# Kernel tuning notes

Measured on AMD Instinct MI355X. Metric: run time of the kernel, lower is better.

## Reference

```python
import jax, jax.numpy as jnp
import numpy as np

N = 50000      # nodes
E = 400000     # edges (avg degree 8)
N_IN = 256     # n_in_chan
N_HID = 256    # n_hid_chan


def gcn_conv(x, src, dst, W, b, n):
    """PyG GCNConv: D^{-1/2}(A+I)D^{-1/2} X W^T + b (add_self_loops=True, unit weights)."""
    h = x @ W.T                                           # [n, out]
    # degree over A + I: each node has a self loop (the initial ones) plus in-edges
    deg = jnp.ones((n,), h.dtype).at[dst].add(1.0)        # [n]
    dinv = jax.lax.rsqrt(deg)                             # deg >= 1 always
    norm = dinv[src] * dinv[dst]                          # [E]
    agg = jnp.zeros_like(h).at[dst].add(h[src] * norm[:, None])
    agg = agg + h * (dinv * dinv)[:, None]                # self-loop term, norm = dinv_i^2
    return agg + b


def setup_inputs() -> dict:
    key = jax.random.key(0)
    k1, k2, k3, k4 = jax.random.split(key, 4)
    x = jax.random.normal(k1, (N, N_IN + N_HID), dtype=jnp.float32)
    edge_index = jax.random.randint(k2, (2, E), 0, N, dtype=jnp.int64)
    s1 = 1.0 / np.sqrt(N_IN + N_HID)
    s2 = 1.0 / np.sqrt(N_HID)
    W1 = jax.random.normal(k3, (N_HID, N_IN + N_HID), dtype=jnp.float32) * s1
    W2 = jax.random.normal(k4, (N_HID, N_HID), dtype=jnp.float32) * s2
    b1 = jnp.zeros((N_HID,), jnp.float32)
    b2 = jnp.zeros((N_HID,), jnp.float32)
    return {"x": x, "edge_index": edge_index, "W1": W1, "b1": b1, "W2": W2, "b2": b2}


def reference(x, edge_index, W1, b1, W2, b2):
    src, dst = edge_index[0], edge_index[1]
    h = jax.nn.relu(gcn_conv(x, src, dst, W1, b1, N))
    return gcn_conv(h, src, dst, W2, b2, N)
```

## Files before the change

### kernel.cpp

```cpp
#include <hip/hip_runtime.h>
#include <hip/hip_bf16.h>

#define NN 50000
#define CH 256
#define SLOTS 96
#define G1K 512
#define G2K 256

typedef unsigned short u16;
typedef unsigned int   u32;

using short8 = __attribute__((ext_vector_type(8))) short;
using u16x8  = __attribute__((ext_vector_type(8))) unsigned short;
using f32x4  = __attribute__((ext_vector_type(4))) float;

static __device__ __forceinline__ float4 ld4(const float* p){ return *(const float4*)p; }

static __device__ __forceinline__ u16 f2b(float f){
  u32 u = __float_as_uint(f);
  u = (u + 0x7fffu + ((u >> 16) & 1u)) >> 16;
  return (u16)u;
}
static __device__ __forceinline__ float b2f(u16 b){
  return __uint_as_float(((u32)b) << 16);
}
static __device__ __forceinline__ int pkbf(float lo, float hi){
  __hip_bfloat162 h = __float22bfloat162_rn(make_float2(lo, hi));
  int r; __builtin_memcpy(&r, &h, 4); return r;
}

static __device__ __forceinline__ void gload_lds16(const u16* g, u16* l){
  __builtin_amdgcn_global_load_lds((const __attribute__((address_space(1))) void*)g,
                                   (__attribute__((address_space(3))) void*)l, 16, 0, 0);
}

#define WBAR(vm) do{ \
    asm volatile("s_waitcnt vmcnt(" #vm ") lgkmcnt(0)" ::: "memory"); \
    __builtin_amdgcn_s_barrier(); \
  }while(0)


__global__ void ell_build_kernel(const int* __restrict__ src, const int* __restrict__ dst,
                                 int* __restrict__ deg, int* __restrict__ ell, int E,
                                 const float* __restrict__ W1, u16* __restrict__ W1bf, int w1n4,
                                 const float* __restrict__ W2, u16* __restrict__ W2bf, int w2n4){
  int T = gridDim.x * 256;
  int g = blockIdx.x*256 + threadIdx.x;
  if (g < E){
    int d = dst[g];
    int pos = atomicAdd(&deg[d], 1);
    if (pos < SLOTS) ell[(size_t)d*SLOTS + pos] = src[g];
  }
  for (int i = g; i < w1n4; i += T){
    float4 v = ld4(W1 + (size_t)i*4);
    ushort4 o; o.x=f2b(v.x); o.y=f2b(v.y); o.z=f2b(v.z); o.w=f2b(v.w);
    *(ushort4*)(W1bf + (size_t)i*4) = o;
  }
  for (int i = g; i < w2n4; i += T){
    float4 v = ld4(W2 + (size_t)i*4);
    ushort4 o; o.x=f2b(v.x); o.y=f2b(v.y); o.z=f2b(v.z); o.w=f2b(v.w);
    *(ushort4*)(W2bf + (size_t)i*4) = o;
  }
}


#define G1_GLB(kt, bb) gload_lds16(gb + (kt)*32, &Bs[bb][wave*512])

#define G1_LA(S, k0) do{ \
    A##S##a = ld4(ga + (k0)); A##S##b = ld4(ga + (k0) + 4); \
  }while(0)

#define G1_SA(S) do{ \
    int4 _w = { pkbf(A##S##a.x,A##S##a.y), pkbf(A##S##a.z,A##S##a.w), \
                pkbf(A##S##b.x,A##S##b.y), pkbf(A##S##b.z,A##S##b.w) }; \
    *(int4*)&As[S][aoff] = _w; \
  }while(0)

#define G1_COMP(ra, rb) do{ \
    short8 af[4], bq[2]; \
    _Pragma("unroll") \
    for (int i=0;i<4;i++) af[i] = *(const short8*)&As[ra][(wm*64 + i*16 + lm)*32 + lk]; \
    _Pragma("unroll") \
    for (int j=0;j<2;j++) bq[j] = *(const short8*)&Bs[rb][(wn*32 + j*16 + lm)*32 + lk]; \
    _Pragma("unroll") \
    for (int i=0;i<4;i++) \
      _Pragma("unroll") \
      for (int j=0;j<2;j++) \
        acc[i][j] = __builtin_amdgcn_mfma_f32_16x16x32_bf16(af[i], bq[j], acc[i][j], 0, 0, 0); \
  }while(0)

__global__ __launch_bounds__(512, 4) void gemm1_kernel(const float* __restrict__ A,
                                                       const u16* __restrict__ Bbf,
                                                       u16* __restrict__ C, int M){
  __shared__ u16 As[2][128*32];
  __shared__ u16 Bs[4][128*32];
  int tid = threadIdx.x;
  int wave = tid >> 6, lane = tid & 63;
  int bm = blockIdx.x, bn = blockIdx.y;

  int sr = tid >> 2;
  int sc = (tid & 3) * 8;
  int ar = bm*128 + sr; if (ar > M-1) ar = M-1;
  const float* ga = A + (size_t)ar*G1K + sc;
  const u16*   gb = Bbf + (size_t)(bn*128 + sr)*G1K + sc;
  int aoff = sr*32 + sc;

  int wm = wave & 1, wn = wave >> 1;
  int lm = lane & 15;
  int lk = (lane >> 4) * 8;

  f32x4 acc[4][2] = {};

  float4 A0a,A0b;
  float4 A1a,A1b;

  G1_LA(0, 0);
  G1_GLB(0, 0);
  G1_LA(1, 32);
  G1_GLB(1, 1);
  G1_SA(0);
  G1_LA(0, 64);
  asm volatile("s_waitcnt vmcnt(0) lgkmcnt(0)" ::: "memory");
  __builtin_amdgcn_s_barrier();

  G1_GLB( 2,2); G1_COMP(0,0); G1_SA(1); G1_LA(1, 96); WBAR(3);
  G1_GLB( 3,3); G1_COMP(1,1); G1_SA(0); G1_LA(0,128); WBAR(3);
  G1_GLB( 4,0); G1_COMP(0,2); G1_SA(1); G1_LA(1,160); WBAR(3);
  G1_GLB( 5,1); G1_COMP(1,3); G1_SA(0); G1_LA(0,192); WBAR(3);
  G1_GLB( 6,2); G1_COMP(0,0); G1_SA(1); G1_LA(1,224); WBAR(3);
  G1_GLB( 7,3); G1_COMP(1,1); G1_SA(0); G1_LA(0,256); WBAR(3);
  G1_GLB( 8,0); G1_COMP(0,2); G1_SA(1); G1_LA(1,288); WBAR(3);
  G1_GLB( 9,1); G1_COMP(1,3); G1_SA(0); G1_LA(0,320); WBAR(3);
  G1_GLB(10,2); G1_COMP(0,0); G1_SA(1); G1_LA(1,352); WBAR(3);
  G1_GLB(11,3); G1_COMP(1,1); G1_SA(0); G1_LA(0,384); WBAR(3);
  G1_GLB(12,0); G1_COMP(0,2); G1_SA(1); G1_LA(1,416); WBAR(3);
  G1_GLB(13,1); G1_COMP(1,3); G1_SA(0); G1_LA(0,448); WBAR(3);
  G1_GLB(14,2); G1_COMP(0,0); G1_SA(1); G1_LA(1,480); WBAR(3);
  G1_GLB(15,3); G1_COMP(1,1); G1_SA(0);               WBAR(1);
                G1_COMP(0,2); G1_SA(1);               WBAR(0);
                G1_COMP(1,3);

  int rb = (lane >> 4) * 4;
  #pragma unroll
  for (int i=0;i<4;i++){
    #pragma unroll
    for (int r=0;r<4;r++){
      int row = bm*128 + wm*64 + i*16 + rb + r;
      if (row < M){
        #pragma unroll
        for (int j=0;j<2;j++){
          int col = bn*128 + wn*32 + j*16 + lm;
          C[(size_t)row*CH + col] = f2b(acc[i][j][r]);
        }
      }
    }
  }
}


#define G2_GLB(kt, bb) do{ \
    gload_lds16(ga + (kt)*32, &As2[bb][wave*512]); \
    gload_lds16(gb + (kt)*32, &Bs2[bb][wave*512]); \
  }while(0)

#define G2_COMP(rb) do{ \
    short8 af[4], bq[2]; \
    _Pragma("unroll") \
    for (int i=0;i<4;i++) af[i] = *(const short8*)&As2[rb][(wm*64 + i*16 + lm)*32 + lk]; \
    _Pragma("unroll") \
    for (int j=0;j<2;j++) bq[j] = *(const short8*)&Bs2[rb][(wn*32 + j*16 + lm)*32 + lk]; \
    _Pragma("unroll") \
    for (int i=0;i<4;i++) \
      _Pragma("unroll") \
      for (int j=0;j<2;j++) \
        acc[i][j] = __builtin_amdgcn_mfma_f32_16x16x32_bf16(af[i], bq[j], acc[i][j], 0, 0, 0); \
  }while(0)

__global__ __launch_bounds__(512, 4) void gemm2_kernel(const u16* __restrict__ A,
                                                       const u16* __restrict__ B,
                                                       u16* __restrict__ C, int M){
  __shared__ u16 As2[4][128*32];
  __shared__ u16 Bs2[4][128*32];
  int tid = threadIdx.x;
  int wave = tid >> 6, lane = tid & 63;
  int bm = blockIdx.x, bn = blockIdx.y;

  int sr = tid >> 2;
  int sc = (tid & 3) * 8;
  int ar = bm*128 + sr; if (ar > M-1) ar = M-1;
  const u16* ga = A + (size_t)ar*G2K + sc;
  const u16* gb = B + (size_t)(bn*128 + sr)*G2K + sc;

  int wm = wave & 1, wn = wave >> 1;
  int lm = lane & 15;
  int lk = (lane >> 4) * 8;

  f32x4 acc[4][2] = {};

  G2_GLB(0, 0);
  G2_GLB(1, 1);
  asm volatile("s_waitcnt vmcnt(0)" ::: "memory");
  __builtin_amdgcn_s_barrier();

  G2_GLB(2, 2); G2_COMP(0); WBAR(2);
  G2_GLB(3, 3); G2_COMP(1); WBAR(2);
  G2_GLB(4, 0); G2_COMP(2); WBAR(2);
  G2_GLB(5, 1); G2_COMP(3); WBAR(2);
  G2_GLB(6, 2); G2_COMP(0); WBAR(2);
  G2_GLB(7, 3); G2_COMP(1); WBAR(2);
                G2_COMP(2); WBAR(0);
                G2_COMP(3);

  int rb = (lane >> 4) * 4;
  #pragma unroll
  for (int i=0;i<4;i++){
    #pragma unroll
    for (int r=0;r<4;r++){
      int row = bm*128 + wm*64 + i*16 + rb + r;
      if (row < M){
        #pragma unroll
        for (int j=0;j<2;j++){
          int col = bn*128 + wn*32 + j*16 + lm;
          C[(size_t)row*CH + col] = f2b(acc[i][j][r]);
        }
      }
    }
  }
}


template<bool RELU, bool OUTBF>
__global__ __launch_bounds__(256) void aggregate_kernel(const u16* __restrict__ h,
                                                        const float* __restrict__ bias,
                                                        const int* __restrict__ deg,
                                                        const int* __restrict__ ell,
                                                        void* __restrict__ outv, int n){
  int wave = threadIdx.x >> 6;
  int lane = threadIdx.x & 63;
  int i = blockIdx.x*4 + wave;
  if (i >= n) return;
  int half = lane >> 5;
  int c = (lane & 31) * 8;

  int degi = deg[i];
  float di = rsqrtf(1.0f + (float)degi);
  int m = degi < SLOTS ? degi : SLOTS;
  const int* row = ell + (size_t)i*SLOTS;

  float acc[8];
  #pragma unroll
  for (int k=0;k<8;k++) acc[k] = 0.f;

  int e = half;
  for (; e + 6 < m; e += 8){
    int s0 = row[e],   s1 = row[e+2], s2 = row[e+4], s3 = row[e+6];
    float n0 = rsqrtf(1.0f + (float)deg[s0]) * di;
    float n1 = rsqrtf(1.0f + (float)deg[s1]) * di;
    float n2 = rsqrtf(1.0f + (float)deg[s2]) * di;
    float n3 = rsqrtf(1.0f + (float)deg[s3]) * di;
    u16x8 h0 = *(const u16x8*)(h + (size_t)s0*CH + c);
    u16x8 h1 = *(const u16x8*)(h + (size_t)s1*CH + c);
    u16x8 h2 = *(const u16x8*)(h + (size_t)s2*CH + c);
    u16x8 h3 = *(const u16x8*)(h + (size_t)s3*CH + c);
    #pragma unroll
    for (int k=0;k<8;k++) acc[k] += b2f(h0[k])*n0;
    #pragma unroll
    for (int k=0;k<8;k++) acc[k] += b2f(h1[k])*n1;
    #pragma unroll
    for (int k=0;k<8;k++) acc[k] += b2f(h2[k])*n2;
    #pragma unroll
    for (int k=0;k<8;k++) acc[k] += b2f(h3[k])*n3;
  }
  for (; e < m; e += 2){
    int s0 = row[e];
    float n0 = rsqrtf(1.0f + (float)deg[s0]) * di;
    u16x8 h0 = *(const u16x8*)(h + (size_t)s0*CH + c);
    #pragma unroll
    for (int k=0;k<8;k++) acc[k] += b2f(h0[k])*n0;
  }

  if (half == 0){
    float w = di*di;
    float4 b0 = ld4(bias + c), b1 = ld4(bias + c + 4);
    u16x8 hv = *(const u16x8*)(h + (size_t)i*CH + c);
    acc[0] += b2f(hv[0])*w + b0.x; acc[1] += b2f(hv[1])*w + b0.y;
    acc[2] += b2f(hv[2])*w + b0.z; acc[3] += b2f(hv[3])*w + b0.w;
    acc[4] += b2f(hv[4])*w + b1.x; acc[5] += b2f(hv[5])*w + b1.y;
    acc[6] += b2f(hv[6])*w + b1.z; acc[7] += b2f(hv[7])*w + b1.w;
  }

  #pragma unroll
  for (int k=0;k<8;k++) acc[k] += __shfl_xor(acc[k], 32, 64);

  if (half == 0){
    if (RELU){
      #pragma unroll
      for (int k=0;k<8;k++) acc[k] = fmaxf(acc[k], 0.f);
    }
    if (OUTBF){
      u16x8 o;
      #pragma unroll
      for (int k=0;k<8;k++) o[k] = f2b(acc[k]);
      *(u16x8*)((u16*)outv + (size_t)i*CH + c) = o;
    } else {
      float* op = (float*)outv + (size_t)i*CH + c;
      *(float4*)op       = make_float4(acc[0],acc[1],acc[2],acc[3]);
      *(float4*)(op + 4) = make_float4(acc[4],acc[5],acc[6],acc[7]);
    }
  }
}


extern "C" void kernel_launch(void* const* d_in, const int* in_sizes, int n_in,
                              void* d_out, int out_size, void* d_ws, size_t ws_size,
                              hipStream_t stream){
  const float* x  = (const float*)d_in[0];
  const int*   ei = (const int*)d_in[1];
  const float* W1 = (const float*)d_in[2];
  const float* b1 = (const float*)d_in[3];
  const float* W2 = (const float*)d_in[4];
  const float* b2 = (const float*)d_in[5];
  float* out = (float*)d_out;

  const int n = NN;
  const int E = in_sizes[1] / 2;
  const int* src = ei;
  const int* dst = ei + E;

  char* ws = (char*)d_ws;
  size_t off = 0;
  auto alloc = [&](size_t bytes)->char* {
    char* p = ws + off;
    off += (bytes + 255) & ~(size_t)255;
    return p;
  };
  u16*   h1bf   = (u16*)  alloc((size_t)n*CH*sizeof(u16));
  u16*   g2out  = (u16*)  alloc((size_t)n*CH*sizeof(u16));
  u16*   W1bf   = (u16*)  alloc((size_t)CH*G1K*sizeof(u16));
  u16*   W2bf   = (u16*)  alloc((size_t)CH*CH*sizeof(u16));
  int*   deg    = (int*)  alloc((size_t)n*sizeof(int));
  int*   ell    = (int*)  alloc((size_t)n*SLOTS*sizeof(int));
  (void)ws_size;

  u16* g1out = (u16*)d_out;

  hipMemsetAsync(deg, 0, (size_t)n*sizeof(int), stream);
  ell_build_kernel<<<(E+255)/256, 256, 0, stream>>>(src, dst, deg, ell, E,
                                                    W1, W1bf, CH*G1K/4,
                                                    W2, W2bf, CH*CH/4);

  dim3 gg((n+127)/128, CH/128);
  gemm1_kernel<<<gg, 512, 0, stream>>>(x, W1bf, g1out, n);
  aggregate_kernel<true, true><<<(n+3)/4, 256, 0, stream>>>(g1out, b1, deg, ell, h1bf, n);

  gemm2_kernel<<<gg, 512, 0, stream>>>(h1bf, W2bf, g2out, n);
  aggregate_kernel<false, false><<<(n+3)/4, 256, 0, stream>>>(g2out, b2, deg, ell, out, n);
}
```

Measured before the change: 313.4 us.

## Retile GEMMs to 64x256 blocks with full-width N per block

```diff
diff --git a/kernel.cpp b/kernel.cpp
--- a/kernel.cpp
+++ b/kernel.cpp
@@ -64,7 +64,12 @@
 }
 
 
-#define G1_GLB(kt, bb) gload_lds16(gb + (kt)*32, &Bs[bb][wave*512])
+#define G1_GLB(kt, bb) do{ \
+    gload_lds16(gB + (size_t)(kt)*32,               &Bs[bb][wave*2048]); \
+    gload_lds16(gB + (size_t)(kt)*32 + 16*G1K,      &Bs[bb][wave*2048 + 512]); \
+    gload_lds16(gB + (size_t)(kt)*32 + 32*G1K,      &Bs[bb][wave*2048 + 1024]); \
+    gload_lds16(gB + (size_t)(kt)*32 + 48*G1K,      &Bs[bb][wave*2048 + 1536]); \
+  }while(0)
 
 #define G1_LA(S, k0) do{ \
     A##S##a = ld4(ga + (k0)); A##S##b = ld4(ga + (k0) + 4); \
@@ -77,79 +82,77 @@
   }while(0)
 
 #define G1_COMP(ra, rb) do{ \
-    short8 af[4], bq[2]; \
-    _Pragma("unroll") \
-    for (int i=0;i<4;i++) af[i] = *(const short8*)&As[ra][(wm*64 + i*16 + lm)*32 + lk]; \
-    _Pragma("unroll") \
-    for (int j=0;j<2;j++) bq[j] = *(const short8*)&Bs[rb][(wn*32 + j*16 + lm)*32 + lk]; \
+    short8 af[4], bq[4]; \
+    _Pragma("unroll") \
+    for (int i=0;i<4;i++) af[i] = *(const short8*)&As[ra][(i*16 + lm)*32 + lk]; \
+    _Pragma("unroll") \
+    for (int j=0;j<4;j++) bq[j] = *(const short8*)&Bs[rb][(wave*64 + j*16 + lm)*32 + lk]; \
     _Pragma("unroll") \
     for (int i=0;i<4;i++) \
       _Pragma("unroll") \
-      for (int j=0;j<2;j++) \
+      for (int j=0;j<4;j++) \
         acc[i][j] = __builtin_amdgcn_mfma_f32_16x16x32_bf16(af[i], bq[j], acc[i][j], 0, 0, 0); \
   }while(0)
 
-__global__ __launch_bounds__(512, 4) void gemm1_kernel(const float* __restrict__ A,
+__global__ __launch_bounds__(256, 4) void gemm1_kernel(const float* __restrict__ A,
                                                        const u16* __restrict__ Bbf,
                                                        u16* __restrict__ C, int M){
-  __shared__ u16 As[2][128*32];
-  __shared__ u16 Bs[4][128*32];
+  __shared__ u16 As[2][64*32];
+  __shared__ u16 Bs[2][256*32];
   int tid = threadIdx.x;
   int wave = tid >> 6, lane = tid & 63;
-  int bm = blockIdx.x, bn = blockIdx.y;
-
-  int sr = tid >> 2;
-  int sc = (tid & 3) * 8;
-  int ar = bm*128 + sr; if (ar > M-1) ar = M-1;
-  const float* ga = A + (size_t)ar*G1K + sc;
-  const u16*   gb = Bbf + (size_t)(bn*128 + sr)*G1K + sc;
-  int aoff = sr*32 + sc;
-
-  int wm = wave & 1, wn = wave >> 1;
+  int bm = blockIdx.x;
+
+  int sra = tid >> 2;
+  int sca = (tid & 3) * 8;
+  int ar = bm*64 + sra; if (ar > M-1) ar = M-1;
+  const float* ga = A + (size_t)ar*G1K + sca;
+  int aoff = sra*32 + sca;
+  const u16* gB = Bbf + (size_t)(wave*64 + (lane>>2))*G1K + (lane&3)*8;
+
   int lm = lane & 15;
   int lk = (lane >> 4) * 8;
 
-  f32x4 acc[4][2] = {};
+  f32x4 acc[4][4] = {};
 
   float4 A0a,A0b;
   float4 A1a,A1b;
 
+  G1_GLB(0, 0);
   G1_LA(0, 0);
-  G1_GLB(0, 0);
   G1_LA(1, 32);
-  G1_GLB(1, 1);
   G1_SA(0);
   G1_LA(0, 64);
   asm volatile("s_waitcnt vmcnt(0) lgkmcnt(0)" ::: "memory");
   __builtin_amdgcn_s_barrier();
 
-  G1_GLB( 2,2); G1_COMP(0,0); G1_SA(1); G1_LA(1, 96); WBAR(3);
-  G1_GLB( 3,3); G1_COMP(1,1); G1_SA(0); G1_LA(0,128); WBAR(3);
-  G1_GLB( 4,0); G1_COMP(0,2); G1_SA(1); G1_LA(1,160); WBAR(3);
-  G1_GLB( 5,1); G1_COMP(1,3); G1_SA(0); G1_LA(0,192); WBAR(3);
-  G1_GLB( 6,2); G1_COMP(0,0); G1_SA(1); G1_LA(1,224); WBAR(3);
-  G1_GLB( 7,3); G1_COMP(1,1); G1_SA(0); G1_LA(0,256); WBAR(3);
-  G1_GLB( 8,0); G1_COMP(0,2); G1_SA(1); G1_LA(1,288); WBAR(3);
-  G1_GLB( 9,1); G1_COMP(1,3); G1_SA(0); G1_LA(0,320); WBAR(3);
-  G1_GLB(10,2); G1_COMP(0,0); G1_SA(1); G1_LA(1,352); WBAR(3);
-  G1_GLB(11,3); G1_COMP(1,1); G1_SA(0); G1_LA(0,384); WBAR(3);
-  G1_GLB(12,0); G1_COMP(0,2); G1_SA(1); G1_LA(1,416); WBAR(3);
-  G1_GLB(13,1); G1_COMP(1,3); G1_SA(0); G1_LA(0,448); WBAR(3);
-  G1_GLB(14,2); G1_COMP(0,0); G1_SA(1); G1_LA(1,480); WBAR(3);
-  G1_GLB(15,3); G1_COMP(1,1); G1_SA(0);               WBAR(1);
-                G1_COMP(0,2); G1_SA(1);               WBAR(0);
-                G1_COMP(1,3);
+  G1_GLB( 1,1); G1_COMP(0,0); G1_SA(1); G1_LA(1, 96); WBAR(2);
+  G1_GLB( 2,0); G1_COMP(1,1); G1_SA(0); G1_LA(0,128); WBAR(2);
+  G1_GLB( 3,1); G1_COMP(0,0); G1_SA(1); G1_LA(1,160); WBAR(2);
+  G1_GLB( 4,0); G1_COMP(1,1); G1_SA(0); G1_LA(0,192); WBAR(2);
+  G1_GLB( 5,1); G1_COMP(0,0); G1_SA(1); G1_LA(1,224); WBAR(2);
+  G1_GLB( 6,0); G1_COMP(1,1); G1_SA(0); G1_LA(0,256); WBAR(2);
+  G1_GLB( 7,1); G1_COMP(0,0); G1_SA(1); G1_LA(1,288); WBAR(2);
+  G1_GLB( 8,0); G1_COMP(1,1); G1_SA(0); G1_LA(0,320); WBAR(2);
+  G1_GLB( 9,1); G1_COMP(0,0); G1_SA(1); G1_LA(1,352); WBAR(2);
+  G1_GLB(10,0); G1_COMP(1,1); G1_SA(0); G1_LA(0,384); WBAR(2);
+  G1_GLB(11,1); G1_COMP(0,0); G1_SA(1); G1_LA(1,416); WBAR(2);
+  G1_GLB(12,0); G1_COMP(1,1); G1_SA(0); G1_LA(0,448); WBAR(2);
+  G1_GLB(13,1); G1_COMP(0,0); G1_SA(1); G1_LA(1,480); WBAR(2);
+  G1_GLB(14,0); G1_COMP(1,1); G1_SA(0);               WBAR(0);
+  G1_GLB(15,1); G1_COMP(0,0); G1_SA(1);               WBAR(0);
+                G1_COMP(1,1);
 
   int rb = (lane >> 4) * 4;
   #pragma unroll
   for (int i=0;i<4;i++){
     #pragma unroll
     for (int r=0;r<4;r++){
-      int row = bm*128 + wm*64 + i*16 + rb + r;
+      int row = bm*64 + i*16 + rb + r;
       if (row < M){
         #pragma unroll
-        for (int j=0;j<2;j++){
-          int col = bn*128 + wn*32 + j*16 + lm;
+        for (int j=0;j<4;j++){
+          int col = wave*64 + j*16 + lm;
           C[(size_t)row*CH + col] = f2b(acc[i][j][r]);
         }
       }
@@ -159,68 +162,67 @@
 
 
 #define G2_GLB(kt, bb) do{ \
-    gload_lds16(ga + (kt)*32, &As2[bb][wave*512]); \
-    gload_lds16(gb + (kt)*32, &Bs2[bb][wave*512]); \
+    gload_lds16(gA + (size_t)(kt)*32,          &As2[bb][wave*512]); \
+    gload_lds16(gB + (size_t)(kt)*32,          &Bs2[bb][wave*2048]); \
+    gload_lds16(gB + (size_t)(kt)*32 + 16*G2K, &Bs2[bb][wave*2048 + 512]); \
+    gload_lds16(gB + (size_t)(kt)*32 + 32*G2K, &Bs2[bb][wave*2048 + 1024]); \
+    gload_lds16(gB + (size_t)(kt)*32 + 48*G2K, &Bs2[bb][wave*2048 + 1536]); \
   }while(0)
 
 #define G2_COMP(rb) do{ \
-    short8 af[4], bq[2]; \
-    _Pragma("unroll") \
-    for (int i=0;i<4;i++) af[i] = *(const short8*)&As2[rb][(wm*64 + i*16 + lm)*32 + lk]; \
-    _Pragma("unroll") \
-    for (int j=0;j<2;j++) bq[j] = *(const short8*)&Bs2[rb][(wn*32 + j*16 + lm)*32 + lk]; \
+    short8 af[4], bq[4]; \
+    _Pragma("unroll") \
+    for (int i=0;i<4;i++) af[i] = *(const short8*)&As2[rb][(i*16 + lm)*32 + lk]; \
+    _Pragma("unroll") \
+    for (int j=0;j<4;j++) bq[j] = *(const short8*)&Bs2[rb][(wave*64 + j*16 + lm)*32 + lk]; \
     _Pragma("unroll") \
     for (int i=0;i<4;i++) \
       _Pragma("unroll") \
-      for (int j=0;j<2;j++) \
+      for (int j=0;j<4;j++) \
         acc[i][j] = __builtin_amdgcn_mfma_f32_16x16x32_bf16(af[i], bq[j], acc[i][j], 0, 0, 0); \
   }while(0)
 
-__global__ __launch_bounds__(512, 4) void gemm2_kernel(const u16* __restrict__ A,
+__global__ __launch_bounds__(256, 4) void gemm2_kernel(const u16* __restrict__ A,
                                                        const u16* __restrict__ B,
                                                        u16* __restrict__ C, int M){
-  __shared__ u16 As2[4][128*32];
-  __shared__ u16 Bs2[4][128*32];
+  __shared__ u16 As2[2][64*32];
+  __shared__ u16 Bs2[2][256*32];
   int tid = threadIdx.x;
   int wave = tid >> 6, lane = tid & 63;
-  int bm = blockIdx.x, bn = blockIdx.y;
-
-  int sr = tid >> 2;
-  int sc = (tid & 3) * 8;
-  int ar = bm*128 + sr; if (ar > M-1) ar = M-1;
-  const u16* ga = A + (size_t)ar*G2K + sc;
-  const u16* gb = B + (size_t)(bn*128 + sr)*G2K + sc;
-
-  int wm = wave & 1, wn = wave >> 1;
+  int bm = blockIdx.x;
+
+  int ar = bm*64 + wave*16 + (lane>>2); if (ar > M-1) ar = M-1;
+  const u16* gA = A + (size_t)ar*G2K + (lane&3)*8;
+  const u16* gB = B + (size_t)(wave*64 + (lane>>2))*G2K + (lane&3)*8;
+
   int lm = lane & 15;
   int lk = (lane >> 4) * 8;
 
-  f32x4 acc[4][2] = {};
+  f32x4 acc[4][4] = {};
 
   G2_GLB(0, 0);
-  G2_GLB(1, 1);
   asm volatile("s_waitcnt vmcnt(0)" ::: "memory");
   __builtin_amdgcn_s_barrier();
 
-  G2_GLB(2, 2); G2_COMP(0); WBAR(2);
-  G2_GLB(3, 3); G2_COMP(1); WBAR(2);
-  G2_GLB(4, 0); G2_COMP(2); WBAR(2);
-  G2_GLB(5, 1); G2_COMP(3); WBAR(2);
-  G2_GLB(6, 2); G2_COMP(0); WBAR(2);
-  G2_GLB(7, 3); G2_COMP(1); WBAR(2);
-                G2_COMP(2); WBAR(0);
-                G2_COMP(3);
+  G2_GLB(1, 1); G2_COMP(0); WBAR(0);
+  G2_GLB(2, 0); G2_COMP(1); WBAR(0);
+  G2_GLB(3, 1); G2_COMP(0); WBAR(0);
+  G2_GLB(4, 0); G2_COMP(1); WBAR(0);
+  G2_GLB(5, 1); G2_COMP(0); WBAR(0);
+  G2_GLB(6, 0); G2_COMP(1); WBAR(0);
+  G2_GLB(7, 1); G2_COMP(0); WBAR(0);
+                G2_COMP(1);
 
   int rb = (lane >> 4) * 4;
   #pragma unroll
   for (int i=0;i<4;i++){
     #pragma unroll
     for (int r=0;r<4;r++){
-      int row = bm*128 + wm*64 + i*16 + rb + r;
+      int row = bm*64 + i*16 + rb + r;
       if (row < M){
         #pragma unroll
-        for (int j=0;j<2;j++){
-          int col = bn*128 + wn*32 + j*16 + lm;
+        for (int j=0;j<4;j++){
+          int col = wave*64 + j*16 + lm;
           C[(size_t)row*CH + col] = f2b(acc[i][j][r]);
         }
       }
@@ -349,10 +351,10 @@
                                                     W1, W1bf, CH*G1K/4,
                                                     W2, W2bf, CH*CH/4);
 
-  dim3 gg((n+127)/128, CH/128);
-  gemm1_kernel<<<gg, 512, 0, stream>>>(x, W1bf, g1out, n);
+  dim3 gg((n+63)/64);
+  gemm1_kernel<<<gg, 256, 0, stream>>>(x, W1bf, g1out, n);
   aggregate_kernel<true, true><<<(n+3)/4, 256, 0, stream>>>(g1out, b1, deg, ell, h1bf, n);
 
-  gemm2_kernel<<<gg, 512, 0, stream>>>(h1bf, W2bf, g2out, n);
+  gemm2_kernel<<<gg, 256, 0, stream>>>(h1bf, W2bf, g2out, n);
   aggregate_kernel<false, false><<<(n+3)/4, 256, 0, stream>>>(g2out, b2, deg, ell, out, n);
 }
```

After: 316.9 us. No clear change (+1.1%).

## Fold degree normalization into GEMM epilogues and aggregate before second GEMM

Applied to the files above, without the earlier changes.

```diff
diff --git a/kernel.cpp b/kernel.cpp
--- a/kernel.cpp
+++ b/kernel.cpp
@@ -29,7 +29,7 @@
   int r; __builtin_memcpy(&r, &h, 4); return r;
 }
 
-static __device__ __forceinline__ void gload_lds16(const u16* g, u16* l){
+static __device__ __forceinline__ void gload_lds16(const void* g, void* l){
   __builtin_amdgcn_global_load_lds((const __attribute__((address_space(1))) void*)g,
                                    (__attribute__((address_space(3))) void*)l, 16, 0, 0);
 }
@@ -53,18 +53,18 @@
   }
   for (int i = g; i < w1n4; i += T){
     float4 v = ld4(W1 + (size_t)i*4);
-    ushort4 o; o.x=f2b(v.x); o.y=f2b(v.y); o.z=f2b(v.z); o.w=f2b(v.w);
-    *(ushort4*)(W1bf + (size_t)i*4) = o;
+    int2 o = { pkbf(v.x,v.y), pkbf(v.z,v.w) };
+    *(int2*)(W1bf + (size_t)i*4) = o;
   }
   for (int i = g; i < w2n4; i += T){
     float4 v = ld4(W2 + (size_t)i*4);
-    ushort4 o; o.x=f2b(v.x); o.y=f2b(v.y); o.z=f2b(v.z); o.w=f2b(v.w);
-    *(ushort4*)(W2bf + (size_t)i*4) = o;
-  }
-}
-
-
-#define G1_GLB(kt, bb) gload_lds16(gb + (kt)*32, &Bs[bb][wave*512])
+    int2 o = { pkbf(v.x,v.y), pkbf(v.z,v.w) };
+    *(int2*)(W2bf + (size_t)i*4) = o;
+  }
+}
+
+
+#define G1_GLB(kt, bb) gload_lds16(gb + (size_t)(kt)*32, &Bs[bb][wave*512])
 
 #define G1_LA(S, k0) do{ \
     A##S##a = ld4(ga + (k0)); A##S##b = ld4(ga + (k0) + 4); \
@@ -91,6 +91,7 @@
 
 __global__ __launch_bounds__(512, 4) void gemm1_kernel(const float* __restrict__ A,
                                                        const u16* __restrict__ Bbf,
+                                                       const int* __restrict__ deg,
                                                        u16* __restrict__ C, int M){
   __shared__ u16 As[2][128*32];
   __shared__ u16 Bs[4][128*32];
@@ -147,10 +148,11 @@
     for (int r=0;r<4;r++){
       int row = bm*128 + wm*64 + i*16 + rb + r;
       if (row < M){
+        float dr = rsqrtf(1.0f + (float)deg[row]);
         #pragma unroll
         for (int j=0;j<2;j++){
           int col = bn*128 + wn*32 + j*16 + lm;
-          C[(size_t)row*CH + col] = f2b(acc[i][j][r]);
+          C[(size_t)row*CH + col] = f2b(acc[i][j][r] * dr);
         }
       }
     }
@@ -159,8 +161,8 @@
 
 
 #define G2_GLB(kt, bb) do{ \
-    gload_lds16(ga + (kt)*32, &As2[bb][wave*512]); \
-    gload_lds16(gb + (kt)*32, &Bs2[bb][wave*512]); \
+    gload_lds16(ga + (size_t)(kt)*32, &As2[bb][wave*512]); \
+    gload_lds16(gb + (size_t)(kt)*32, &Bs2[bb][wave*512]); \
   }while(0)
 
 #define G2_COMP(rb) do{ \
@@ -178,7 +180,8 @@
 
 __global__ __launch_bounds__(512, 4) void gemm2_kernel(const u16* __restrict__ A,
                                                        const u16* __restrict__ B,
-                                                       u16* __restrict__ C, int M){
+                                                       float* __restrict__ Cout,
+                                                       const float* __restrict__ bias, int M){
   __shared__ u16 As2[4][128*32];
   __shared__ u16 Bs2[4][128*32];
   int tid = threadIdx.x;
@@ -210,6 +213,10 @@
   G2_GLB(7, 3); G2_COMP(1); WBAR(2);
                 G2_COMP(2); WBAR(0);
                 G2_COMP(3);
+
+  float bv[2];
+  #pragma unroll
+  for (int j=0;j<2;j++) bv[j] = bias[bn*128 + wn*32 + j*16 + lm];
 
   int rb = (lane >> 4) * 4;
   #pragma unroll
@@ -221,7 +228,7 @@
         #pragma unroll
         for (int j=0;j<2;j++){
           int col = bn*128 + wn*32 + j*16 + lm;
-          C[(size_t)row*CH + col] = f2b(acc[i][j][r]);
+          Cout[(size_t)row*CH + col] = acc[i][j][r] + bv[j];
         }
       }
     }
@@ -229,85 +236,85 @@
 }
 
 
-template<bool RELU, bool OUTBF>
+#define AGG_G(u, s) ushort4 hg##u = *(const ushort4*)(h + (size_t)(s)*CH + c)
+#define AGG_ACC(u) do{ a0 += b2f(hg##u.x); a1 += b2f(hg##u.y); \
+                       a2 += b2f(hg##u.z); a3 += b2f(hg##u.w); }while(0)
+
+template<bool RELU, bool BIAS, bool SCALEOUT>
 __global__ __launch_bounds__(256) void aggregate_kernel(const u16* __restrict__ h,
                                                         const float* __restrict__ bias,
                                                         const int* __restrict__ deg,
                                                         const int* __restrict__ ell,
-                                                        void* __restrict__ outv, int n){
+                                                        u16* __restrict__ outv, int n){
   int wave = threadIdx.x >> 6;
   int lane = threadIdx.x & 63;
   int i = blockIdx.x*4 + wave;
   if (i >= n) return;
-  int half = lane >> 5;
-  int c = (lane & 31) * 8;
+  i = __builtin_amdgcn_readfirstlane(i);
 
   int degi = deg[i];
   float di = rsqrtf(1.0f + (float)degi);
   int m = degi < SLOTS ? degi : SLOTS;
-  const int* row = ell + (size_t)i*SLOTS;
-
-  float acc[8];
-  #pragma unroll
-  for (int k=0;k<8;k++) acc[k] = 0.f;
-
-  int e = half;
-  for (; e + 6 < m; e += 8){
-    int s0 = row[e],   s1 = row[e+2], s2 = row[e+4], s3 = row[e+6];
-    float n0 = rsqrtf(1.0f + (float)deg[s0]) * di;
-    float n1 = rsqrtf(1.0f + (float)deg[s1]) * di;
-    float n2 = rsqrtf(1.0f + (float)deg[s2]) * di;
-    float n3 = rsqrtf(1.0f + (float)deg[s3]) * di;
-    u16x8 h0 = *(const u16x8*)(h + (size_t)s0*CH + c);
-    u16x8 h1 = *(const u16x8*)(h + (size_t)s1*CH + c);
-    u16x8 h2 = *(const u16x8*)(h + (size_t)s2*CH + c);
-    u16x8 h3 = *(const u16x8*)(h + (size_t)s3*CH + c);
-    #pragma unroll
-    for (int k=0;k<8;k++) acc[k] += b2f(h0[k])*n0;
-    #pragma unroll
-    for (int k=0;k<8;k++) acc[k] += b2f(h1[k])*n1;
-    #pragma unroll
-    for (int k=0;k<8;k++) acc[k] += b2f(h2[k])*n2;
-    #pragma unroll
-    for (int k=0;k<8;k++) acc[k] += b2f(h3[k])*n3;
-  }
-  for (; e < m; e += 2){
-    int s0 = row[e];
-    float n0 = rsqrtf(1.0f + (float)deg[s0]) * di;
-    u16x8 h0 = *(const u16x8*)(h + (size_t)s0*CH + c);
-    #pragma unroll
-    for (int k=0;k<8;k++) acc[k] += b2f(h0[k])*n0;
-  }
-
-  if (half == 0){
-    float w = di*di;
-    float4 b0 = ld4(bias + c), b1 = ld4(bias + c + 4);
-    u16x8 hv = *(const u16x8*)(h + (size_t)i*CH + c);
-    acc[0] += b2f(hv[0])*w + b0.x; acc[1] += b2f(hv[1])*w + b0.y;
-    acc[2] += b2f(hv[2])*w + b0.z; acc[3] += b2f(hv[3])*w + b0.w;
-    acc[4] += b2f(hv[4])*w + b1.x; acc[5] += b2f(hv[5])*w + b1.y;
-    acc[6] += b2f(hv[6])*w + b1.z; acc[7] += b2f(hv[7])*w + b1.w;
-  }
-
-  #pragma unroll
-  for (int k=0;k<8;k++) acc[k] += __shfl_xor(acc[k], 32, 64);
-
-  if (half == 0){
-    if (RELU){
-      #pragma unroll
-      for (int k=0;k<8;k++) acc[k] = fmaxf(acc[k], 0.f);
-    }
-    if (OUTBF){
-      u16x8 o;
-      #pragma unroll
-      for (int k=0;k<8;k++) o[k] = f2b(acc[k]);
-      *(u16x8*)((u16*)outv + (size_t)i*CH + c) = o;
-    } else {
-      float* op = (float*)outv + (size_t)i*CH + c;
-      *(float4*)op       = make_float4(acc[0],acc[1],acc[2],acc[3]);
-      *(float4*)(op + 4) = make_float4(acc[4],acc[5],acc[6],acc[7]);
-    }
-  }
+  const int* __restrict__ row = ell + (size_t)i*SLOTS;
+  int vidx = row[lane];
+  int c = lane * 4;
+
+  float a0=0.f, a1=0.f, a2=0.f, a3=0.f;
+
+  int m64 = m < 64 ? m : 64;
+  int nb = m64 >> 3;
+  for (int b = 0; b < nb; ++b){
+    int base = b*8;
+    int s0=__shfl(vidx,base  ), s1=__shfl(vidx,base+1), s2=__shfl(vidx,base+2), s3=__shfl(vidx,base+3);
+    int s4=__shfl(vidx,base+4), s5=__shfl(vidx,base+5), s6=__shfl(vidx,base+6), s7=__shfl(vidx,base+7);
+    AGG_G(0,s0); AGG_G(1,s1); AGG_G(2,s2); AGG_G(3,s3);
+    AGG_G(4,s4); AGG_G(5,s5); AGG_G(6,s6); AGG_G(7,s7);
+    AGG_ACC(0); AGG_ACC(1); AGG_ACC(2); AGG_ACC(3);
+    AGG_ACC(4); AGG_ACC(5); AGG_ACC(6); AGG_ACC(7);
+  }
+  int base = nb*8;
+  if (base < m64){
+    int t0 = base   < m64 ? __shfl(vidx,base  ) : i;  float w0 = base   < m64 ? 1.f : 0.f;
+    int t1 = base+1 < m64 ? __shfl(vidx,base+1) : i;  float w1 = base+1 < m64 ? 1.f : 0.f;
+    int t2 = base+2 < m64 ? __shfl(vidx,base+2) : i;  float w2 = base+2 < m64 ? 1.f : 0.f;
+    int t3 = base+3 < m64 ? __shfl(vidx,base+3) : i;  float w3 = base+3 < m64 ? 1.f : 0.f;
+    int t4 = base+4 < m64 ? __shfl(vidx,base+4) : i;  float w4 = base+4 < m64 ? 1.f : 0.f;
+    int t5 = base+5 < m64 ? __shfl(vidx,base+5) : i;  float w5 = base+5 < m64 ? 1.f : 0.f;
+    int t6 = base+6 < m64 ? __shfl(vidx,base+6) : i;  float w6 = base+6 < m64 ? 1.f : 0.f;
+    int t7 = base+7 < m64 ? __shfl(vidx,base+7) : i;  float w7 = base+7 < m64 ? 1.f : 0.f;
+    AGG_G(0,t0); AGG_G(1,t1); AGG_G(2,t2); AGG_G(3,t3);
+    AGG_G(4,t4); AGG_G(5,t5); AGG_G(6,t6); AGG_G(7,t7);
+    a0 += b2f(hg0.x)*w0 + b2f(hg1.x)*w1 + b2f(hg2.x)*w2 + b2f(hg3.x)*w3
+        + b2f(hg4.x)*w4 + b2f(hg5.x)*w5 + b2f(hg6.x)*w6 + b2f(hg7.x)*w7;
+    a1 += b2f(hg0.y)*w0 + b2f(hg1.y)*w1 + b2f(hg2.y)*w2 + b2f(hg3.y)*w3
+        + b2f(hg4.y)*w4 + b2f(hg5.y)*w5 + b2f(hg6.y)*w6 + b2f(hg7.y)*w7;
+    a2 += b2f(hg0.z)*w0 + b2f(hg1.z)*w1 + b2f(hg2.z)*w2 + b2f(hg3.z)*w3
+        + b2f(hg4.z)*w4 + b2f(hg5.z)*w5 + b2f(hg6.z)*w6 + b2f(hg7.z)*w7;
+    a3 += b2f(hg0.w)*w0 + b2f(hg1.w)*w1 + b2f(hg2.w)*w2 + b2f(hg3.w)*w3
+        + b2f(hg4.w)*w4 + b2f(hg5.w)*w5 + b2f(hg6.w)*w6 + b2f(hg7.w)*w7;
+  }
+  for (int e = 64; e < m; ++e){
+    int s = row[e];
+    ushort4 hv = *(const ushort4*)(h + (size_t)s*CH + c);
+    a0 += b2f(hv.x); a1 += b2f(hv.y); a2 += b2f(hv.z); a3 += b2f(hv.w);
+  }
+
+  ushort4 hv = *(const ushort4*)(h + (size_t)i*CH + c);
+  a0 += b2f(hv.x); a1 += b2f(hv.y); a2 += b2f(hv.z); a3 += b2f(hv.w);
+
+  float v0 = a0*di, v1 = a1*di, v2 = a2*di, v3 = a3*di;
+  if (BIAS){
+    float4 b = ld4(bias + c);
+    v0 += b.x; v1 += b.y; v2 += b.z; v3 += b.w;
+  }
+  if (RELU){
+    v0 = fmaxf(v0, 0.f); v1 = fmaxf(v1, 0.f);
+    v2 = fmaxf(v2, 0.f); v3 = fmaxf(v3, 0.f);
+  }
+  if (SCALEOUT){ v0 *= di; v1 *= di; v2 *= di; v3 *= di; }
+
+  ushort4 o; o.x = f2b(v0); o.y = f2b(v1); o.z = f2b(v2); o.w = f2b(v3);
+  *(ushort4*)(outv + (size_t)i*CH + c) = o;
 }
 
 
@@ -335,7 +342,7 @@
     return p;
   };
   u16*   h1bf   = (u16*)  alloc((size_t)n*CH*sizeof(u16));
-  u16*   g2out  = (u16*)  alloc((size_t)n*CH*sizeof(u16));
+  u16*   h2bf   = (u16*)  alloc((size_t)n*CH*sizeof(u16));
   u16*   W1bf   = (u16*)  alloc((size_t)CH*G1K*sizeof(u16));
   u16*   W2bf   = (u16*)  alloc((size_t)CH*CH*sizeof(u16));
   int*   deg    = (int*)  alloc((size_t)n*sizeof(int));
@@ -350,9 +357,10 @@
                                                     W2, W2bf, CH*CH/4);
 
   dim3 gg((n+127)/128, CH/128);
-  gemm1_kernel<<<gg, 512, 0, stream>>>(x, W1bf, g1out, n);
-  aggregate_kernel<true, true><<<(n+3)/4, 256, 0, stream>>>(g1out, b1, deg, ell, h1bf, n);
-
-  gemm2_kernel<<<gg, 512, 0, stream>>>(h1bf, W2bf, g2out, n);
-  aggregate_kernel<false, false><<<(n+3)/4, 256, 0, stream>>>(g2out, b2, deg, ell, out, n);
-}
+
+  gemm1_kernel<<<gg, 512, 0, stream>>>(x, W1bf, deg, g1out, n);
+  aggregate_kernel<true, true, true><<<(n+3)/4, 256, 0, stream>>>(g1out, b1, deg, ell, h1bf, n);
+
+  aggregate_kernel<false, false, false><<<(n+3)/4, 256, 0, stream>>>(h1bf, b2, deg, ell, h2bf, n);
+  gemm2_kernel<<<gg, 512, 0, stream>>>(h2bf, W2bf, out, b2, n);
+}
```

Result: no change. 312.6 us (-0.2%).
